# Kernel optimization log

Hardware: AMD Instinct MI355X
Metric: run time of the kernel (lower is better)

## Reference

```python
import jax, jax.numpy as jnp
import numpy as np

B, N, DIM = 4, 4096, 1024
HEADS, DIM_HEAD, BSZ, EPS = 8, 64, 16, 1e-8
INNER = HEADS * DIM_HEAD


def setup_inputs() -> dict:
    key = jax.random.key(0)
    k1, k2, k3 = jax.random.split(key, 3)
    x = jax.random.normal(k1, (B, N, DIM), dtype=jnp.float32)
    # torch nn.Linear weights are [out, in]; scale ~ fan_in^-0.5 for stable exp()
    w_qkv = jax.random.normal(k2, (3 * INNER, DIM), dtype=jnp.float32) * (DIM ** -0.5)
    w_out = jax.random.normal(k3, (DIM, INNER), dtype=jnp.float32) * (INNER ** -0.5)
    b_out = jnp.zeros((DIM,), dtype=jnp.float32)
    return {"x": x, "w_qkv": w_qkv, "w_out": w_out, "b_out": b_out}


def _to_bh(t, b, n):
    # 'b n (h d) -> (b h) n d'
    return t.reshape(b, n, HEADS, DIM_HEAD).transpose(0, 2, 1, 3).reshape(b * HEADS, n, DIM_HEAD)


def _to_blocks(t):
    # 'b (n z) d -> b n z d'
    return t.reshape(t.shape[0], -1, BSZ, DIM_HEAD)


def _calc_Y_and_A(qb, kb, vb):
    S = jnp.einsum('bnid,bnjd->bnij', qb, kb)   # block-local scores
    A = jnp.exp(S)
    y = jnp.einsum('bnij,bnjd->bnid', A, vb)
    return y.reshape(y.shape[0], -1, DIM_HEAD), A.sum(-1).reshape(A.shape[0], -1)


def _hattention(x, w_qkv, w_out, b_out):
    b, n, _ = x.shape
    qkv = x @ w_qkv.T
    q, k, v = jnp.split(qkv, 3, axis=-1)
    q, k, v = (_to_bh(t, b, n) for t in (q, k, v))
    q = q * (DIM_HEAD ** -0.5)

    num_levels = int(np.log2(n // BSZ)) - 1
    qkvs = [(q, k, v)]
    for _ in range(num_levels):
        q = q.reshape(q.shape[0], -1, 2, DIM_HEAD).mean(axis=2)
        k = k.reshape(k.shape[0], -1, 2, DIM_HEAD).mean(axis=2)
        v = v.reshape(v.shape[0], -1, 2, DIM_HEAD).sum(axis=2)
        qkvs.append((q, k, v))
    top_level = qkvs[0]
    coarse_levels = qkvs[1:][::-1]  # coarsest first

    Ys = []
    for (ql, kl, vl) in coarse_levels:
        qb, kb, vb = map(_to_blocks, (ql, kl, vl))
        bh, nb = kb.shape[0], kb.shape[1]
        # flip sibling key blocks: 'b (n r) z d' with r=2 reversed
        kb = kb.reshape(bh, nb // 2, 2, BSZ, DIM_HEAD)[:, :, ::-1].reshape(bh, nb, BSZ, DIM_HEAD)
        Ys.append(_calc_Y_and_A(qb, kb, vb))
    Ys.append(_calc_Y_and_A(*map(_to_blocks, top_level)))

    Y, A = Ys[0]
    for y_l, a_l in Ys[1:]:
        Y = jnp.repeat(Y, 2, axis=1) + y_l
        A = jnp.repeat(A, 2, axis=1) + a_l

    out = Y / (A + EPS)[..., None]
    # '(b h) n d -> b n (h d)'
    out = out.reshape(b, HEADS, n, DIM_HEAD).transpose(0, 2, 1, 3).reshape(b, n, INNER)
    return out @ w_out.T + b_out


def reference(x, w_qkv, w_out, b_out):
    return _hattention(x, w_qkv, w_out, b_out)
```

## Files before the change

kernel.cpp:

```cpp
#include <hip/hip_runtime.h>
#include <hip/hip_bf16.h>


typedef __bf16 bf16x8 __attribute__((ext_vector_type(8)));
typedef float floatx4 __attribute__((ext_vector_type(4)));
typedef unsigned short ushortx8 __attribute__((ext_vector_type(8)));
typedef unsigned int uintx4 __attribute__((ext_vector_type(4)));

#define ROWS_PER_BH 8160

__device__ __forceinline__ void g2lds16(const void* g, void* l) {
  __builtin_amdgcn_global_load_lds(
      (const __attribute__((address_space(1))) void*)g,
      (__attribute__((address_space(3))) void*)l, 16, 0, 0);
}

__device__ __forceinline__ unsigned short f2bu(float x) {
  __hip_bfloat16 h = __float2bfloat16(x);
  return *(unsigned short*)&h;
}
__device__ __forceinline__ float bu2f(unsigned short u) {
  __hip_bfloat16 h = *(__hip_bfloat16*)&u;
  return __bfloat162float(h);
}

__device__ __forceinline__ void wg_barrier() {
  asm volatile("" ::: "memory");
  __builtin_amdgcn_s_barrier();
  asm volatile("" ::: "memory");
}
__device__ __forceinline__ void lgk0() {
  asm volatile("s_waitcnt lgkmcnt(0)" ::: "memory");
}

__global__ __launch_bounds__(256) void f2b_kernel(const float* __restrict__ s,
                                                  __hip_bfloat16* __restrict__ d,
                                                  int n) {
  int i0 = (blockIdx.x * 256 + threadIdx.x) * 4;
  if (i0 + 3 < n) {
    float4 v = *(const float4*)(s + i0);
    d[i0 + 0] = __float2bfloat16(v.x);
    d[i0 + 1] = __float2bfloat16(v.y);
    d[i0 + 2] = __float2bfloat16(v.z);
    d[i0 + 3] = __float2bfloat16(v.w);
  }
}

template <int K>
__device__ __forceinline__ void gemm256_core(const unsigned short* __restrict__ A,
                                             const unsigned short* __restrict__ B,
                                             unsigned short* lds, int tM, int tN,
                                             floatx4 acc[8][4]) {
  const int tid = threadIdx.x;
  const int lane = tid & 63;
  const int w = tid >> 6;
  const int wm = w >> 2, wn = w & 3;

  const int srow = tid >> 3;
  const int schunk = (tid & 7) ^ (srow & 7);
  const unsigned short* Ab = A + (size_t)(tM + srow) * K + schunk * 8;
  const unsigned short* Bb = B + (size_t)(tN + srow) * K + schunk * 8;
  const int ltid8 = tid * 8;

  auto stage = [&](const unsigned short* gbase, unsigned short* lbase, int half, int kt) {
    const unsigned short* g = gbase + (size_t)(half * 128) * K + kt;
    unsigned short* l = lbase + half * 8192 + ltid8;
    g2lds16(g, l);
    g2lds16(g + (size_t)64 * K, l + 4096);
  };

  stage(Ab, lds, 0, 0); stage(Ab, lds, 1, 0);
  stage(Bb, lds + 16384, 0, 0); stage(Bb, lds + 16384, 1, 0);
  stage(Ab, lds + 32768, 0, 64); stage(Ab, lds + 32768, 1, 64);
  stage(Bb, lds + 49152, 0, 64); stage(Bb, lds + 49152, 1, 64);
  asm volatile("s_waitcnt vmcnt(8)" ::: "memory");
  wg_barrier();

  const int frow = lane & 15, quad = lane >> 4, sw = frow & 7;
  const int arbase = (wm * 128 + frow) * 64;
  const int brbase = (wn * 64 + frow) * 64;
  const int NT = K / 64;

  for (int t = 0; t < NT; ++t) {
    unsigned short* lA = lds + ((t & 1) << 15);
    unsigned short* lB = lA + 16384;
    const int ktn = (t + 2) * 64;
    const bool st = (t + 2) < NT;

    bf16x8 bfr[4][2], a01[2][2][2];
#pragma unroll
    for (int nf = 0; nf < 4; nf++)
#pragma unroll
      for (int kk = 0; kk < 2; kk++)
        bfr[nf][kk] = *(const bf16x8*)&lB[brbase + nf * 1024 + (((kk * 4 + quad) ^ sw) * 8)];
#pragma unroll
    for (int q = 0; q < 2; q++)
#pragma unroll
      for (int mf2 = 0; mf2 < 2; mf2++)
#pragma unroll
        for (int kk = 0; kk < 2; kk++)
          a01[q][mf2][kk] = *(const bf16x8*)&lA[arbase + (q * 2 + mf2) * 1024 +
                                                (((kk * 4 + quad) ^ sw) * 8)];
    wg_barrier();
    lgk0();
    __builtin_amdgcn_s_setprio(1);
#pragma unroll
    for (int mf2 = 0; mf2 < 2; mf2++)
#pragma unroll
      for (int nf = 0; nf < 4; nf++)
#pragma unroll
        for (int kk = 0; kk < 2; kk++)
          acc[mf2][nf] = __builtin_amdgcn_mfma_f32_16x16x32_bf16(
              a01[0][mf2][kk], bfr[nf][kk], acc[mf2][nf], 0, 0, 0);
    __builtin_amdgcn_s_setprio(0);
    wg_barrier();

    bf16x8 a23[2][2][2];
#pragma unroll
    for (int q = 0; q < 2; q++)
#pragma unroll
      for (int mf2 = 0; mf2 < 2; mf2++)
#pragma unroll
        for (int kk = 0; kk < 2; kk++)
          a23[q][mf2][kk] = *(const bf16x8*)&lA[arbase + (4 + q * 2 + mf2) * 1024 +
                                                (((kk * 4 + quad) ^ sw) * 8)];
    if (st) { stage(Bb, lB, 0, ktn); stage(Bb, lB, 1, ktn); }
    wg_barrier();
    lgk0();
    __builtin_amdgcn_s_setprio(1);
#pragma unroll
    for (int mf2 = 0; mf2 < 2; mf2++)
#pragma unroll
      for (int nf = 0; nf < 4; nf++)
#pragma unroll
        for (int kk = 0; kk < 2; kk++)
          acc[2 + mf2][nf] = __builtin_amdgcn_mfma_f32_16x16x32_bf16(
              a01[1][mf2][kk], bfr[nf][kk], acc[2 + mf2][nf], 0, 0, 0);
    __builtin_amdgcn_s_setprio(0);
    wg_barrier();

    if (st) stage(Ab, lA, 0, ktn);
    wg_barrier();
    __builtin_amdgcn_s_setprio(1);
#pragma unroll
    for (int mf2 = 0; mf2 < 2; mf2++)
#pragma unroll
      for (int nf = 0; nf < 4; nf++)
#pragma unroll
        for (int kk = 0; kk < 2; kk++)
          acc[4 + mf2][nf] = __builtin_amdgcn_mfma_f32_16x16x32_bf16(
              a23[0][mf2][kk], bfr[nf][kk], acc[4 + mf2][nf], 0, 0, 0);
    __builtin_amdgcn_s_setprio(0);
    wg_barrier();

    if (st) stage(Ab, lA, 1, ktn);
    wg_barrier();
    __builtin_amdgcn_s_setprio(1);
#pragma unroll
    for (int mf2 = 0; mf2 < 2; mf2++)
#pragma unroll
      for (int nf = 0; nf < 4; nf++)
#pragma unroll
        for (int kk = 0; kk < 2; kk++)
          acc[6 + mf2][nf] = __builtin_amdgcn_mfma_f32_16x16x32_bf16(
              a23[1][mf2][kk], bfr[nf][kk], acc[6 + mf2][nf], 0, 0, 0);
    __builtin_amdgcn_s_setprio(0);
    if (st) asm volatile("s_waitcnt vmcnt(6)" ::: "memory");
    else    asm volatile("s_waitcnt vmcnt(0)" ::: "memory");
    wg_barrier();
  }
}

__global__ __launch_bounds__(512, 2) void gemm_qkv_kernel(
    const unsigned short* __restrict__ A,
    const unsigned short* __restrict__ B,
    __hip_bfloat16* __restrict__ qp, __hip_bfloat16* __restrict__ kp,
    __hip_bfloat16* __restrict__ vp) {
  __shared__ __align__(16) unsigned short lds[65536];
  const int lane = threadIdx.x & 63, w = threadIdx.x >> 6;
  const int wm = w >> 2, wn = w & 3;
  const int tM = blockIdx.x * 256, tN = blockIdx.y * 256;

  floatx4 acc[8][4];
#pragma unroll
  for (int i = 0; i < 8; i++)
#pragma unroll
    for (int j = 0; j < 4; j++) acc[i][j] = (floatx4){0.f, 0.f, 0.f, 0.f};

  gemm256_core<1024>(A, B, lds, tM, tN, acc);

  const int quad = lane >> 4, m15 = lane & 15;
  const int cbase = tN + wn * 64;
  const int tensor = cbase >> 9;
  const int h = (cbase & 511) >> 6;
  __hip_bfloat16* dstbuf = (tensor == 0) ? qp : ((tensor == 1) ? kp : vp);
  const float scale = (tensor == 0) ? 0.125f : 1.0f;
#pragma unroll
  for (int mf = 0; mf < 8; mf++) {
#pragma unroll
    for (int nf = 0; nf < 4; nf++) {
#pragma unroll
      for (int r = 0; r < 4; r++) {
        const int m = tM + wm * 128 + mf * 16 + quad * 4 + r;
        const int b = m >> 12, n = m & 4095;
        dstbuf[((size_t)(b * 8 + h) * ROWS_PER_BH + n) * 64 + nf * 16 + m15] =
            __float2bfloat16(acc[mf][nf][r] * scale);
      }
    }
  }
}

__global__ __launch_bounds__(512, 2) void gemm_out_kernel(
    const unsigned short* __restrict__ A,
    const unsigned short* __restrict__ B,
    const float* __restrict__ bias, float* __restrict__ out) {
  __shared__ __align__(16) unsigned short lds[65536];
  const int lane = threadIdx.x & 63, w = threadIdx.x >> 6;
  const int wm = w >> 2, wn = w & 3;
  const int tM = blockIdx.x * 256, tN = blockIdx.y * 256;

  floatx4 acc[8][4];
#pragma unroll
  for (int i = 0; i < 8; i++)
#pragma unroll
    for (int j = 0; j < 4; j++) acc[i][j] = (floatx4){0.f, 0.f, 0.f, 0.f};

  gemm256_core<512>(A, B, lds, tM, tN, acc);

  const int quad = lane >> 4, m15 = lane & 15;
#pragma unroll
  for (int mf = 0; mf < 8; mf++) {
#pragma unroll
    for (int nf = 0; nf < 4; nf++) {
      const int c = tN + wn * 64 + nf * 16 + m15;
      const float bb = bias[c];
#pragma unroll
      for (int r = 0; r < 4; r++) {
        const int m = tM + wm * 128 + mf * 16 + quad * 4 + r;
        out[(size_t)m * 1024 + c] = acc[mf][nf][r] + bb;
      }
    }
  }
}

__global__ __launch_bounds__(256) void pyramid_all_kernel(
    __hip_bfloat16* __restrict__ qp, __hip_bfloat16* __restrict__ kp,
    __hip_bfloat16* __restrict__ vp) {
  __shared__ unsigned short qs[128 * 64], ks[128 * 64], vs[128 * 64];
  const int bh = blockIdx.x >> 5;
  const int chunk = blockIdx.x & 31;
  const int tid = threadIdx.x;
  const size_t base = (size_t)bh * ROWS_PER_BH;
  const size_t g0 = (base + chunk * 128) * 64;
  const unsigned short* qg = (const unsigned short*)qp;
  const unsigned short* kg = (const unsigned short*)kp;
  const unsigned short* vg = (const unsigned short*)vp;
#pragma unroll
  for (int c = 0; c < 4; c++) {
    int off = c * 2048 + tid * 8;
    *(ushortx8*)&qs[off] = *(const ushortx8*)(qg + g0 + off);
    *(ushortx8*)&ks[off] = *(const ushortx8*)(kg + g0 + off);
    *(ushortx8*)&vs[off] = *(const ushortx8*)(vg + g0 + off);
  }
  const int offs[8] = {0, 4096, 6144, 7168, 7680, 7936, 8064, 8128};
#pragma unroll
  for (int l = 1; l <= 7; l++) {
    __syncthreads();
    const int nOut = 128 >> l;
    for (int e = tid; e < nOut * 32; e += 256) {
      const int i = e >> 5, dp = (e & 31) * 2;
      const int a = (i << l) * 64 + dp;
      const int b = a + (1 << (l - 1)) * 64;
      unsigned short q0 = f2bu(0.5f * (bu2f(qs[a]) + bu2f(qs[b])));
      unsigned short q1 = f2bu(0.5f * (bu2f(qs[a + 1]) + bu2f(qs[b + 1])));
      unsigned short k0 = f2bu(0.5f * (bu2f(ks[a]) + bu2f(ks[b])));
      unsigned short k1 = f2bu(0.5f * (bu2f(ks[a + 1]) + bu2f(ks[b + 1])));
      unsigned short v0 = f2bu(bu2f(vs[a]) + bu2f(vs[b]));
      unsigned short v1 = f2bu(bu2f(vs[a + 1]) + bu2f(vs[b + 1]));
      qs[a] = q0; qs[a + 1] = q1;
      ks[a] = k0; ks[a + 1] = k1;
      vs[a] = v0; vs[a + 1] = v1;
      const size_t grow = (base + offs[l] + (size_t)chunk * nOut + i) * 64 + dp;
      *(unsigned int*)((unsigned short*)qp + grow) = (unsigned int)q0 | ((unsigned int)q1 << 16);
      *(unsigned int*)((unsigned short*)kp + grow) = (unsigned int)k0 | ((unsigned int)k1 << 16);
      *(unsigned int*)((unsigned short*)vp + grow) = (unsigned int)v0 | ((unsigned int)v1 << 16);
    }
  }
}

__global__ __launch_bounds__(256) void attn_kernel(
    const unsigned short* __restrict__ qp, const unsigned short* __restrict__ kp,
    const unsigned short* __restrict__ vp, __hip_bfloat16* __restrict__ yall,
    float* __restrict__ aall) {
  __shared__ __align__(16) unsigned short vT[4][64 * 24];
  const int w = threadIdx.x >> 6, lane = threadIdx.x & 63;
  const int g = blockIdx.x * 4 + w;
  if (g >= 510) return;
  const int bh = blockIdx.y;
  int level, blk;
  if (g < 256)      { level = 0; blk = g; }
  else if (g < 384) { level = 1; blk = g - 256; }
  else if (g < 448) { level = 2; blk = g - 384; }
  else if (g < 480) { level = 3; blk = g - 448; }
  else if (g < 496) { level = 4; blk = g - 480; }
  else if (g < 504) { level = 5; blk = g - 496; }
  else if (g < 508) { level = 6; blk = g - 504; }
  else              { level = 7; blk = g - 508; }
  const int ro = 8192 - (8192 >> level);
  const int kblk = (level == 0) ? blk : (blk ^ 1);
  const int m = lane & 15, q = lane >> 4;
  const size_t qbase = ((size_t)bh * ROWS_PER_BH + ro + blk * 16) * 64;
  const size_t kbase = ((size_t)bh * ROWS_PER_BH + ro + kblk * 16) * 64;

  const bf16x8 ka0 = *(const bf16x8*)(kp + kbase + m * 64 + q * 8);
  const bf16x8 ka1 = *(const bf16x8*)(kp + kbase + m * 64 + 32 + q * 8);
  const bf16x8 qb0 = *(const bf16x8*)(qp + qbase + m * 64 + q * 8);
  const bf16x8 qb1 = *(const bf16x8*)(qp + qbase + m * 64 + 32 + q * 8);

  const ushortx8 v0 = *(const ushortx8*)(vp + qbase + m * 64 + q * 16);
  const ushortx8 v1 = *(const ushortx8*)(vp + qbase + m * 64 + q * 16 + 8);
  unsigned short* vtw = vT[w];
#pragma unroll
  for (int j = 0; j < 8; j++) vtw[(q * 16 + j) * 24 + m] = v0[j];
#pragma unroll
  for (int j = 0; j < 8; j++) vtw[(q * 16 + 8 + j) * 24 + m] = v1[j];

  floatx4 s = (floatx4){0.f, 0.f, 0.f, 0.f};
  s = __builtin_amdgcn_mfma_f32_16x16x32_bf16(ka0, qb0, s, 0, 0, 0);
  s = __builtin_amdgcn_mfma_f32_16x16x32_bf16(ka1, qb1, s, 0, 0, 0);

  unsigned short pb0 = f2bu(__expf(s[0])), pb1 = f2bu(__expf(s[1]));
  unsigned short pb2 = f2bu(__expf(s[2])), pb3 = f2bu(__expf(s[3]));
  float asum = bu2f(pb0) + bu2f(pb1) + bu2f(pb2) + bu2f(pb3);
  asum += __shfl_xor(asum, 16, 64);
  asum += __shfl_xor(asum, 32, 64);
  const size_t arow = (size_t)bh * ROWS_PER_BH + ro + blk * 16;
  if (q == 0) aall[arow + m] = asum;

  unsigned int d0 = (unsigned int)pb0 | ((unsigned int)pb1 << 16);
  unsigned int d1 = (unsigned int)pb2 | ((unsigned int)pb3 << 16);
  const int s0l = m + 32 * (q & 1);
  unsigned int u0 = __shfl(d0, s0l, 64);
  unsigned int u1 = __shfl(d1, s0l, 64);
  unsigned int u2 = __shfl(d0, s0l + 16, 64);
  unsigned int u3 = __shfl(d1, s0l + 16, 64);
  union { uintx4 i; bf16x8 b; } pau;
  pau.i = (q < 2) ? (uintx4){u0, u1, u2, u3} : (uintx4){0u, 0u, 0u, 0u};
  const bf16x8 pa = pau.b;

#pragma unroll
  for (int c = 0; c < 4; c++) {
    union { uintx4 i; bf16x8 b; } bvu;
    bvu.i = (uintx4){0u, 0u, 0u, 0u};
    if (q < 2) bvu.b = *(const bf16x8*)&vtw[(c * 16 + m) * 24 + q * 8];
    floatx4 y = (floatx4){0.f, 0.f, 0.f, 0.f};
    y = __builtin_amdgcn_mfma_f32_16x16x32_bf16(pa, bvu.b, y, 0, 0, 0);
#pragma unroll
    for (int r = 0; r < 4; r++)
      yall[(arow + q * 4 + r) * 64 + c * 16 + m] = __float2bfloat16(y[r]);
  }
}

__global__ __launch_bounds__(256) void combine_kernel(
    const unsigned short* __restrict__ yall, const float* __restrict__ aall,
    __hip_bfloat16* __restrict__ Ub) {
  int idx = blockIdx.x * 256 + threadIdx.x;
  int d = idx & 63;
  int i = (idx >> 6) & 4095;
  int bh = idx >> 18;
  size_t base = (size_t)bh * ROWS_PER_BH;
  float Y = 0.f, Aa = 0.f;
#pragma unroll
  for (int l = 0; l < 8; l++) {
    int r = (8192 - (8192 >> l)) + (i >> l);
    Y += bu2f(yall[(base + r) * 64 + d]);
    Aa += aall[base + r];
  }
  float u = Y / (Aa + 1e-8f);
  int b = bh >> 3, h = bh & 7;
  size_t m = (size_t)b * 4096 + i;
  Ub[m * 512 + (size_t)h * 64 + d] = __float2bfloat16(u);
}

extern "C" void kernel_launch(void* const* d_in, const int* in_sizes, int n_in,
                              void* d_out, int out_size, void* d_ws, size_t ws_size,
                              hipStream_t stream) {
  const float* x     = (const float*)d_in[0];
  const float* w_qkv = (const float*)d_in[1];
  const float* w_out = (const float*)d_in[2];
  const float* b_out = (const float*)d_in[3];
  float* out = (float*)d_out;

  char* ws = (char*)d_ws;
  __hip_bfloat16* xb    = (__hip_bfloat16*)(ws + 0);
  __hip_bfloat16* wqkvb = (__hip_bfloat16*)(ws + 33554432);
  __hip_bfloat16* wob   = (__hip_bfloat16*)(ws + 36700160);
  __hip_bfloat16* qp    = (__hip_bfloat16*)(ws + 37748736);
  __hip_bfloat16* kp    = (__hip_bfloat16*)(ws + 71172096);
  __hip_bfloat16* vp    = (__hip_bfloat16*)(ws + 104595456);
  __hip_bfloat16* yall  = (__hip_bfloat16*)(ws + 138018816);
  float* aall           = (float*)(ws + 171442176);
  __hip_bfloat16* Ub    = (__hip_bfloat16*)(ws + 172486656);

  f2b_kernel<<<16384, 256, 0, stream>>>(x, xb, 16777216);
  f2b_kernel<<<1536, 256, 0, stream>>>(w_qkv, wqkvb, 1572864);
  f2b_kernel<<<512, 256, 0, stream>>>(w_out, wob, 524288);

  gemm_qkv_kernel<<<dim3(64, 6), 512, 0, stream>>>(
      (const unsigned short*)xb, (const unsigned short*)wqkvb, qp, kp, vp);

  pyramid_all_kernel<<<1024, 256, 0, stream>>>(qp, kp, vp);

  attn_kernel<<<dim3(128, 32), 256, 0, stream>>>(
      (const unsigned short*)qp, (const unsigned short*)kp,
      (const unsigned short*)vp, yall, aall);

  combine_kernel<<<32768, 256, 0, stream>>>((const unsigned short*)yall, aall, Ub);

  gemm_out_kernel<<<dim3(64, 4), 512, 0, stream>>>(
      (const unsigned short*)Ub, (const unsigned short*)wob, b_out, out);
}
```

Before: 285.6 us.

## Restructure GEMM mainloop to split K into halves and shorten A-tile prefetch distance

```diff
diff --git a/kernel.cpp b/kernel.cpp
--- a/kernel.cpp
+++ b/kernel.cpp
@@ -71,102 +71,100 @@
 
   stage(Ab, lds, 0, 0); stage(Ab, lds, 1, 0);
   stage(Bb, lds + 16384, 0, 0); stage(Bb, lds + 16384, 1, 0);
-  stage(Ab, lds + 32768, 0, 64); stage(Ab, lds + 32768, 1, 64);
   stage(Bb, lds + 49152, 0, 64); stage(Bb, lds + 49152, 1, 64);
-  asm volatile("s_waitcnt vmcnt(8)" ::: "memory");
+  asm volatile("s_waitcnt vmcnt(4)" ::: "memory");
   wg_barrier();
 
   const int frow = lane & 15, quad = lane >> 4, sw = frow & 7;
   const int arbase = (wm * 128 + frow) * 64;
   const int brbase = (wn * 64 + frow) * 64;
+  const int c0 = (quad ^ sw) * 8;
+  const int c1 = ((4 + quad) ^ sw) * 8;
   const int NT = K / 64;
 
   for (int t = 0; t < NT; ++t) {
     unsigned short* lA = lds + ((t & 1) << 15);
     unsigned short* lB = lA + 16384;
-    const int ktn = (t + 2) * 64;
-    const bool st = (t + 2) < NT;
-
-    bf16x8 bfr[4][2], a01[2][2][2];
+    unsigned short* nA = lds + (((t + 1) & 1) << 15);
+    const bool stA = (t + 1) < NT;
+    const bool stB = (t + 2) < NT;
+    const int ktA = (t + 1) * 64, ktB = (t + 2) * 64;
+
+    bf16x8 bfr[4], af[4], ag[4];
+
 #pragma unroll
     for (int nf = 0; nf < 4; nf++)
-#pragma unroll
-      for (int kk = 0; kk < 2; kk++)
-        bfr[nf][kk] = *(const bf16x8*)&lB[brbase + nf * 1024 + (((kk * 4 + quad) ^ sw) * 8)];
-#pragma unroll
-    for (int q = 0; q < 2; q++)
-#pragma unroll
-      for (int mf2 = 0; mf2 < 2; mf2++)
-#pragma unroll
-        for (int kk = 0; kk < 2; kk++)
-          a01[q][mf2][kk] = *(const bf16x8*)&lA[arbase + (q * 2 + mf2) * 1024 +
-                                                (((kk * 4 + quad) ^ sw) * 8)];
+      bfr[nf] = *(const bf16x8*)&lB[brbase + nf * 1024 + c0];
+#pragma unroll
+    for (int mf = 0; mf < 4; mf++)
+      af[mf] = *(const bf16x8*)&lA[arbase + mf * 1024 + c0];
+    if (stA) stage(Ab, nA, 0, ktA);
     wg_barrier();
     lgk0();
     __builtin_amdgcn_s_setprio(1);
 #pragma unroll
-    for (int mf2 = 0; mf2 < 2; mf2++)
+    for (int mf = 0; mf < 4; mf++)
 #pragma unroll
       for (int nf = 0; nf < 4; nf++)
-#pragma unroll
-        for (int kk = 0; kk < 2; kk++)
-          acc[mf2][nf] = __builtin_amdgcn_mfma_f32_16x16x32_bf16(
-              a01[0][mf2][kk], bfr[nf][kk], acc[mf2][nf], 0, 0, 0);
+        acc[mf][nf] = __builtin_amdgcn_mfma_f32_16x16x32_bf16(
+            af[mf], bfr[nf], acc[mf][nf], 0, 0, 0);
     __builtin_amdgcn_s_setprio(0);
     wg_barrier();
 
-    bf16x8 a23[2][2][2];
-#pragma unroll
-    for (int q = 0; q < 2; q++)
-#pragma unroll
-      for (int mf2 = 0; mf2 < 2; mf2++)
-#pragma unroll
-        for (int kk = 0; kk < 2; kk++)
-          a23[q][mf2][kk] = *(const bf16x8*)&lA[arbase + (4 + q * 2 + mf2) * 1024 +
-                                                (((kk * 4 + quad) ^ sw) * 8)];
-    if (st) { stage(Bb, lB, 0, ktn); stage(Bb, lB, 1, ktn); }
+#pragma unroll
+    for (int mf = 0; mf < 4; mf++)
+      ag[mf] = *(const bf16x8*)&lA[arbase + (4 + mf) * 1024 + c0];
+    if (stA) stage(Ab, nA, 1, ktA);
     wg_barrier();
     lgk0();
     __builtin_amdgcn_s_setprio(1);
 #pragma unroll
-    for (int mf2 = 0; mf2 < 2; mf2++)
+    for (int mf = 0; mf < 4; mf++)
 #pragma unroll
       for (int nf = 0; nf < 4; nf++)
-#pragma unroll
-        for (int kk = 0; kk < 2; kk++)
-          acc[2 + mf2][nf] = __builtin_amdgcn_mfma_f32_16x16x32_bf16(
-              a01[1][mf2][kk], bfr[nf][kk], acc[2 + mf2][nf], 0, 0, 0);
+        acc[4 + mf][nf] = __builtin_amdgcn_mfma_f32_16x16x32_bf16(
+            ag[mf], bfr[nf], acc[4 + mf][nf], 0, 0, 0);
     __builtin_amdgcn_s_setprio(0);
     wg_barrier();
 
-    if (st) stage(Ab, lA, 0, ktn);
-    wg_barrier();
+#pragma unroll
+    for (int nf = 0; nf < 4; nf++)
+      bfr[nf] = *(const bf16x8*)&lB[brbase + nf * 1024 + c1];
+#pragma unroll
+    for (int mf = 0; mf < 4; mf++)
+      af[mf] = *(const bf16x8*)&lA[arbase + mf * 1024 + c1];
+    wg_barrier();
+    lgk0();
     __builtin_amdgcn_s_setprio(1);
 #pragma unroll
-    for (int mf2 = 0; mf2 < 2; mf2++)
+    for (int mf = 0; mf < 4; mf++)
 #pragma unroll
       for (int nf = 0; nf < 4; nf++)
-#pragma unroll
-        for (int kk = 0; kk < 2; kk++)
-          acc[4 + mf2][nf] = __builtin_amdgcn_mfma_f32_16x16x32_bf16(
-              a23[0][mf2][kk], bfr[nf][kk], acc[4 + mf2][nf], 0, 0, 0);
+        acc[mf][nf] = __builtin_amdgcn_mfma_f32_16x16x32_bf16(
+            af[mf], bfr[nf], acc[mf][nf], 0, 0, 0);
     __builtin_amdgcn_s_setprio(0);
     wg_barrier();
 
-    if (st) stage(Ab, lA, 1, ktn);
-    wg_barrier();
+#pragma unroll
+    for (int mf = 0; mf < 4; mf++)
+      ag[mf] = *(const bf16x8*)&lA[arbase + (4 + mf) * 1024 + c1];
+    if (stB) {
+      stage(Bb, lB, 0, ktB);
+      stage(Bb, lB, 1, ktB);
+      asm volatile("s_waitcnt vmcnt(4)" ::: "memory");
+    } else {
+      asm volatile("s_waitcnt vmcnt(0)" ::: "memory");
+    }
+    wg_barrier();
+    lgk0();
     __builtin_amdgcn_s_setprio(1);
 #pragma unroll
-    for (int mf2 = 0; mf2 < 2; mf2++)
+    for (int mf = 0; mf < 4; mf++)
 #pragma unroll
       for (int nf = 0; nf < 4; nf++)
-#pragma unroll
-        for (int kk = 0; kk < 2; kk++)
-          acc[6 + mf2][nf] = __builtin_amdgcn_mfma_f32_16x16x32_bf16(
-              a23[1][mf2][kk], bfr[nf][kk], acc[6 + mf2][nf], 0, 0, 0);
+        acc[4 + mf][nf] = __builtin_amdgcn_mfma_f32_16x16x32_bf16(
+            ag[mf], bfr[nf], acc[4 + mf][nf], 0, 0, 0);
     __builtin_amdgcn_s_setprio(0);
-    if (st) asm volatile("s_waitcnt vmcnt(6)" ::: "memory");
-    else    asm volatile("s_waitcnt vmcnt(0)" ::: "memory");
     wg_barrier();
   }
 }
```

Result: no change. 283.8 us (-0.6%).
